# Optimization experiments

Measured on AMD Instinct MI355X. Metric: run time of the kernel, lower is better.

Reference implementation:

```python
import jax, jax.numpy as jnp
import numpy as np

B, S, D = 4, 4096, 2048
DH = D // 2
EPS = 1e-6


def setup_inputs() -> dict:
    key = jax.random.key(0)
    ks = jax.random.split(key, 6)
    return {
        "inputs": jax.random.normal(ks[0], (B * S, D), jnp.float32),
        "lf1_cache": jax.random.normal(ks[1], (B, D, 1, 1), jnp.float32),
        "lf2_cache": jax.random.normal(ks[2], (B, DH, 1, 1), jnp.float32),
        "w1": jax.random.normal(ks[3], (DH, D, 2), jnp.float32) / np.sqrt(2.0 * D).astype(np.float32),
        "b1": jnp.zeros((DH,), jnp.float32),
        "w2": jax.random.normal(ks[4], (D, DH, 2), jnp.float32) / np.sqrt(2.0 * DH).astype(np.float32),
        "b2": jnp.zeros((D,), jnp.float32),
        "ln_w": jnp.ones((D,), jnp.float32),
    }


def reference(inputs, lf1_cache, lf2_cache, w1, b1, w2, b2, ln_w):
    # inputs: [B*S, D] flat tokens; caches hold one previous timestep per batch.
    x = inputs.reshape(B, S, D)
    # prepend cached timestep -> [B, S+1, D]  (equiv. to torch.cat along conv time dim)
    x_cat = jnp.concatenate([lf1_cache[:, :, 0, 0][:, None, :], x], axis=1)
    # conv1: kernel size 2 over time, dense over channels (groups=1)
    # o1[b,t,e] = sum_d w1[e,d,0]*x_cat[b,t,d] + w1[e,d,1]*x_cat[b,t+1,d] + b1[e]
    o1 = (jnp.einsum('btd,ed->bte', x_cat[:, :-1], w1[:, :, 0])
          + jnp.einsum('btd,ed->bte', x_cat[:, 1:], w1[:, :, 1]) + b1)  # [B,S,DH]
    o1_cat = jnp.concatenate([lf2_cache[:, :, 0, 0][:, None, :], o1], axis=1)  # [B,S+1,DH]
    o2 = (jnp.einsum('bte,de->btd', o1_cat[:, :-1], w2[:, :, 0])
          + jnp.einsum('bte,de->btd', o1_cat[:, 1:], w2[:, :, 1]) + b2)  # [B,S,D]
    y = o2 + x  # residual add
    # RMSNorm over the channel dim
    inv_rms = jax.lax.rsqrt(jnp.mean(y * y, axis=-1, keepdims=True) + EPS)
    lf_output = y * inv_rms * ln_w  # [B, S, D]
    # new caches: last timestep of conv1 input and conv2 input, in [B,C,1,1] layout
    lf1 = x_cat[:, -1][:, :, None, None]
    lf2 = o1_cat[:, -1][:, :, None, None]
    return lf_output, lf1, lf2
```

## Files before the change

### kernel.cpp

```cpp
#include <hip/hip_runtime.h>
#include <cstdint>

#define BB 4
#define SS 4096
#define DD 2048
#define DH 1024
#define MM (BB * SS)
#define EPSV 1e-6f

typedef unsigned short u16;
typedef __bf16 bf16x8 __attribute__((ext_vector_type(8)));
typedef float f32x4 __attribute__((ext_vector_type(4)));


__device__ __forceinline__ u16 f2bf(float f) {
    uint32_t u = __float_as_uint(f);
    u += 0x7fffu + ((u >> 16) & 1u);
    return (u16)(u >> 16);
}

__device__ __forceinline__ void async16(const void* g, void* l) {
    __builtin_amdgcn_global_load_lds(
        (const __attribute__((address_space(1))) uint32_t*)g,
        (__attribute__((address_space(3))) uint32_t*)l,
        16, 0, 0);
}

#define FENCE asm volatile("" ::: "memory")


__global__ void cvt_f32_bf16(const float* __restrict__ in, u16* __restrict__ out, long n4) {
    long i = (long)blockIdx.x * blockDim.x + threadIdx.x;
    if (i >= n4) return;
    float4 v = *(const float4*)(in + i * 4);
    ushort4 o;
    o.x = f2bf(v.x); o.y = f2bf(v.y); o.z = f2bf(v.z); o.w = f2bf(v.w);
    *(ushort4*)(out + i * 4) = o;
}

__global__ void pack_w(const float* __restrict__ in, u16* __restrict__ out, int dshift) {
    int idx = blockIdx.x * 256 + threadIdx.x;
    int Dd = 1 << dshift;
    int e = idx >> dshift;
    int d = idx & (Dd - 1);
    float2 v = *(const float2*)(in + (long)idx * 2);
    long rowbase = (long)e * (Dd * 2);
    out[rowbase + d] = f2bf(v.x);
    out[rowbase + Dd + d] = f2bf(v.y);
}

template <int KD, int MODE>
__launch_bounds__(512, 2)
__global__ void gemm2tap(const u16* __restrict__ A,
                         const u16* __restrict__ cache,
                         const u16* __restrict__ Bt,
                         const float* __restrict__ bias,
                         u16* __restrict__ obf,
                         float* __restrict__ lf2out,
                         const float* __restrict__ xres,
                         float* __restrict__ yout)
{
    constexpr int KTOT = 2 * KD;
    constexpr int NT = KTOT / 64;
    constexpr int HALF_T = NT / 2;
    constexpr int NN = (MODE == 1) ? DH : DD;
    static_assert(NT >= 4 && (NT & 1) == 0, "tile schedule needs even NT >= 4");

    const int tid = threadIdx.x;
    const int lane = tid & 63;
    const int wave = tid >> 6;
    const int bm = blockIdx.x;
    const int bn = blockIdx.y;

    __shared__ __align__(16) u16 sm[65536];

    const int srow = wave * 16 + (lane >> 2);
    const int skc  = (lane & 3) ^ ((lane >> 3) & 3);
    const int sRowA = wave * 512;

    const u16 *aPrev0, *aPrev1, *aCur0, *aCur1, *bPtr0, *bPtr1;
    {
        long r0 = (long)bm * 256 + srow;
        long r1 = r0 + 128;
        aCur0 = A + r0 * KD + skc * 8;
        aCur1 = A + r1 * KD + skc * 8;
        aPrev0 = ((((int)r0) & (SS - 1)) == 0) ? (cache + (r0 >> 12) * KD + skc * 8)
                                               : (A + (r0 - 1) * KD + skc * 8);
        aPrev1 = ((((int)r1) & (SS - 1)) == 0) ? (cache + (r1 >> 12) * KD + skc * 8)
                                               : (A + (r1 - 1) * KD + skc * 8);
        long n0l = (long)bn * 256 + srow;
        bPtr0 = Bt + n0l * KTOT + skc * 8;
        bPtr1 = Bt + (n0l + 128) * KTOT + skc * 8;
    }

#define STAGE_A(DBUF_, TT_, KS_) do {                                          \
        const int _ko = (TT_) * 64 + (KS_) * 32;                               \
        const u16 *_g0, *_g1;                                                  \
        if ((TT_) < HALF_T) { _g0 = aPrev0 + _ko; _g1 = aPrev1 + _ko; }        \
        else { _g0 = aCur0 + (_ko - KD); _g1 = aCur1 + (_ko - KD); }           \
        async16(_g0, sm + (DBUF_) * 32768 + (KS_) * 8192 + sRowA);             \
        async16(_g1, sm + (DBUF_) * 32768 + (KS_) * 8192 + 4096 + sRowA);      \
    } while (0)

#define STAGE_B(DBUF_, TT_, KS_) do {                                          \
        const int _ko = (TT_) * 64 + (KS_) * 32;                               \
        async16(bPtr0 + _ko, sm + (DBUF_) * 32768 + 16384 + (KS_) * 8192 + sRowA);        \
        async16(bPtr1 + _ko, sm + (DBUF_) * 32768 + 16384 + (KS_) * 8192 + 4096 + sRowA); \
    } while (0)

    const int frow = lane & 15;
    const int fquad = lane >> 4;
    const int wm128 = (wave >> 2) * 128;
    const int wn64  = (wave & 3) * 64;
    const int fq8s = (fquad ^ ((frow >> 1) & 3)) * 8;
    const int afb = (wm128 + frow) * 32 + fq8s;
    const int bfb = (wn64 + frow) * 32 + fq8s;

    f32x4 acc[8][4];
#pragma unroll
    for (int i = 0; i < 8; ++i)
#pragma unroll
        for (int j = 0; j < 4; ++j)
            acc[i][j] = (f32x4){0.f, 0.f, 0.f, 0.f};

#define MFMA_(D_, A_, B_) D_ = __builtin_amdgcn_mfma_f32_16x16x32_bf16(A_, B_, D_, 0, 0, 0)

#define TILE2(T_, DB_, SP0_, SP1_, VM0S_, VM1S_)                               \
  {                                                                            \
    const u16* aro = sm + (DB_) * 32768;                                       \
    const u16* bro = aro + 16384;                                              \
    bf16x8 af[8], bq[4];                                                       \
                                   \
    _Pragma("unroll")                                                          \
    for (int mf = 0; mf < 8; ++mf)                                             \
        af[mf] = *(const bf16x8*)(aro + afb + mf * 512);                       \
    _Pragma("unroll")                                                          \
    for (int nf = 0; nf < 4; ++nf)                                             \
        bq[nf] = *(const bf16x8*)(bro + bfb + nf * 512);                       \
    if (SP0_) { STAGE_A((DB_) ^ 1, (T_) + 1, 1); STAGE_B((DB_) ^ 1, (T_) + 1, 1); } \
    FENCE; __builtin_amdgcn_s_barrier(); FENCE;                                \
    __builtin_amdgcn_s_setprio(1);                                             \
    _Pragma("unroll")                                                          \
    for (int mf = 0; mf < 8; ++mf)                                             \
        _Pragma("unroll")                                                      \
        for (int nf = 0; nf < 4; ++nf)                                         \
            MFMA_(acc[mf][nf], af[mf], bq[nf]);                                \
    __builtin_amdgcn_s_setprio(0);                                             \
    asm volatile(VM0S_ ::: "memory");                                          \
    __builtin_amdgcn_s_barrier(); FENCE;                                       \
                                   \
    _Pragma("unroll")                                                          \
    for (int mf = 0; mf < 8; ++mf)                                             \
        af[mf] = *(const bf16x8*)(aro + 8192 + afb + mf * 512);                \
    _Pragma("unroll")                                                          \
    for (int nf = 0; nf < 4; ++nf)                                             \
        bq[nf] = *(const bf16x8*)(bro + 8192 + bfb + nf * 512);                \
    if (SP1_) { STAGE_A((DB_), (T_) + 2, 0); STAGE_B((DB_), (T_) + 2, 0); }    \
    FENCE; __builtin_amdgcn_s_barrier(); FENCE;                                \
    __builtin_amdgcn_s_setprio(1);                                             \
    _Pragma("unroll")                                                          \
    for (int mf = 0; mf < 8; ++mf)                                             \
        _Pragma("unroll")                                                      \
        for (int nf = 0; nf < 4; ++nf)                                         \
            MFMA_(acc[mf][nf], af[mf], bq[nf]);                                \
    __builtin_amdgcn_s_setprio(0);                                             \
    asm volatile(VM1S_ ::: "memory");                                          \
    __builtin_amdgcn_s_barrier(); FENCE;                                       \
  }

    STAGE_A(0, 0, 0);
    STAGE_B(0, 0, 0);
    FENCE;
    STAGE_A(0, 0, 1);
    STAGE_B(0, 0, 1);
    STAGE_A(1, 1, 0);
    STAGE_B(1, 1, 0);
    asm volatile("s_waitcnt vmcnt(8)" ::: "memory");
    __builtin_amdgcn_s_barrier(); FENCE;

    for (int t = 0; t < NT - 2; t += 2) {
        TILE2(t,     0, 1, 1, "s_waitcnt vmcnt(8)", "s_waitcnt vmcnt(8)");
        TILE2(t + 1, 1, 1, 1, "s_waitcnt vmcnt(8)", "s_waitcnt vmcnt(8)");
    }
    TILE2(NT - 2, 0, 1, 0, "s_waitcnt vmcnt(8)", "s_waitcnt vmcnt(4)");
    TILE2(NT - 1, 1, 0, 0, "s_waitcnt vmcnt(0)", "s_waitcnt vmcnt(0)");

#undef TILE2
#undef STAGE_A
#undef STAGE_B

    const long m0 = (long)bm * 256 + wm128;
    const int n0 = bn * 256 + wn64;
#pragma unroll
    for (int mf = 0; mf < 8; ++mf) {
#pragma unroll
        for (int nf = 0; nf < 4; ++nf) {
            const int n = n0 + nf * 16 + frow;
            const float bv = bias[n];
#pragma unroll
            for (int v = 0; v < 4; ++v) {
                const long m = m0 + mf * 16 + fquad * 4 + v;
                float val = acc[mf][nf][v] + bv;
                if (MODE == 1) {
                    obf[m * NN + n] = f2bf(val);
                    if ((((int)m) & (SS - 1)) == (SS - 1))
                        lf2out[(m >> 12) * NN + n] = val;
                } else {
                    val += xres[m * NN + n];
                    yout[m * NN + n] = val;
                }
            }
        }
    }
}


__global__ void rmsnorm_inplace(float* __restrict__ y, const float* __restrict__ lnw) {
    const long r = blockIdx.x;
    float* row = y + r * DD;
    const int tid = threadIdx.x;

    float4 v0 = *(float4*)(row + tid * 4);
    float4 v1 = *(float4*)(row + 1024 + tid * 4);
    float s = v0.x * v0.x + v0.y * v0.y + v0.z * v0.z + v0.w * v0.w
            + v1.x * v1.x + v1.y * v1.y + v1.z * v1.z + v1.w * v1.w;
#pragma unroll
    for (int off = 32; off; off >>= 1) s += __shfl_xor(s, off, 64);

    __shared__ float red[4];
    if ((tid & 63) == 0) red[tid >> 6] = s;
    __syncthreads();
    float tot = red[0] + red[1] + red[2] + red[3];
    float inv = rsqrtf(tot * (1.0f / DD) + EPSV);

    float4 w0 = *(const float4*)(lnw + tid * 4);
    float4 w1 = *(const float4*)(lnw + 1024 + tid * 4);
    v0.x *= inv * w0.x; v0.y *= inv * w0.y; v0.z *= inv * w0.z; v0.w *= inv * w0.w;
    v1.x *= inv * w1.x; v1.y *= inv * w1.y; v1.z *= inv * w1.z; v1.w *= inv * w1.w;
    *(float4*)(row + tid * 4) = v0;
    *(float4*)(row + 1024 + tid * 4) = v1;
}

__global__ void lf1_copy(const float* __restrict__ x, float* __restrict__ out) {
    int idx = blockIdx.x * 256 + threadIdx.x;
    int b = idx >> 11;
    int d = idx & (DD - 1);
    out[idx] = x[((long)b * SS + (SS - 1)) * DD + d];
}


extern "C" void kernel_launch(void* const* d_in, const int* in_sizes, int n_in,
                              void* d_out, int out_size, void* d_ws, size_t ws_size,
                              hipStream_t stream) {
    const float* x    = (const float*)d_in[0];
    const float* lf1c = (const float*)d_in[1];
    const float* lf2c = (const float*)d_in[2];
    const float* w1   = (const float*)d_in[3];
    const float* b1   = (const float*)d_in[4];
    const float* w2   = (const float*)d_in[5];
    const float* b2   = (const float*)d_in[6];
    const float* lnw  = (const float*)d_in[7];

    float* out    = (float*)d_out;
    float* lf1out = out + (long)MM * DD;
    float* lf2out = lf1out + (long)BB * DD;

    char* ws = (char*)d_ws;
    u16* Xbf  = (u16*)ws; ws += (long)MM * DD * 2;
    u16* o1bf = (u16*)ws; ws += (long)MM * DH * 2;
    u16* W1b  = (u16*)ws; ws += (long)DH * (2 * DD) * 2;
    u16* W2b  = (u16*)ws; ws += (long)DD * (2 * DH) * 2;
    u16* c1   = (u16*)ws; ws += (long)BB * DD * 2;
    u16* c2   = (u16*)ws; ws += (long)BB * DH * 2;

    cvt_f32_bf16<<<32768, 256, 0, stream>>>(x, Xbf, (long)MM * DD / 4);
    cvt_f32_bf16<<<8, 256, 0, stream>>>(lf1c, c1, (long)BB * DD / 4);
    cvt_f32_bf16<<<4, 256, 0, stream>>>(lf2c, c2, (long)BB * DH / 4);
    pack_w<<<(DH * DD) / 256, 256, 0, stream>>>(w1, W1b, 11);
    pack_w<<<(DD * DH) / 256, 256, 0, stream>>>(w2, W2b, 10);

    gemm2tap<DD, 1><<<dim3(MM / 256, DH / 256), 512, 0, stream>>>(
        Xbf, c1, W1b, b1, o1bf, lf2out, nullptr, nullptr);

    gemm2tap<DH, 2><<<dim3(MM / 256, DD / 256), 512, 0, stream>>>(
        o1bf, c2, W2b, b2, nullptr, nullptr, x, out);

    rmsnorm_inplace<<<MM, 256, 0, stream>>>(out, lnw);
    lf1_copy<<<BB * DD / 256, 256, 0, stream>>>(x, lf1out);
}
```

Baseline: 571.0 us.

## Replace double-buffered K tiles with 4-slot ring pipeline, one barrier per step

Restructures the GEMM main loop from two 64-wide K tiles, each split into two 32-wide halves with two barriers per half, into a 4-slot ring of 32-wide K substeps. Each substep prefetches three substeps ahead and synchronises with a single barrier. This is meant to cut barrier count and deepen prefetch so more global-load latency hides behind MFMA work. It relies on careful vmcnt accounting; a wrong wait count could race on LDS slots.

```diff
diff --git a/kernel.cpp b/kernel.cpp
--- a/kernel.cpp
+++ b/kernel.cpp
@@ -62,9 +62,9 @@
 {
     constexpr int KTOT = 2 * KD;
     constexpr int NT = KTOT / 64;
-    constexpr int HALF_T = NT / 2;
+    constexpr int NS = 2 * NT;
     constexpr int NN = (MODE == 1) ? DH : DD;
-    static_assert(NT >= 4 && (NT & 1) == 0, "tile schedule needs even NT >= 4");
+    static_assert(NS % 4 == 0 && NS >= 8, "ring-4 schedule needs NS % 4 == 0, NS >= 8");
 
     const int tid = threadIdx.x;
     const int lane = tid & 63;
@@ -93,19 +93,15 @@
         bPtr1 = Bt + (n0l + 128) * KTOT + skc * 8;
     }
 
-#define STAGE_A(DBUF_, TT_, KS_) do {                                          \
-        const int _ko = (TT_) * 64 + (KS_) * 32;                               \
+#define STAGE(SLOT_, U_) do {                                                  \
+        const int _u = (U_);                                                   \
         const u16 *_g0, *_g1;                                                  \
-        if ((TT_) < HALF_T) { _g0 = aPrev0 + _ko; _g1 = aPrev1 + _ko; }        \
-        else { _g0 = aCur0 + (_ko - KD); _g1 = aCur1 + (_ko - KD); }           \
-        async16(_g0, sm + (DBUF_) * 32768 + (KS_) * 8192 + sRowA);             \
-        async16(_g1, sm + (DBUF_) * 32768 + (KS_) * 8192 + 4096 + sRowA);      \
-    } while (0)
-
-#define STAGE_B(DBUF_, TT_, KS_) do {                                          \
-        const int _ko = (TT_) * 64 + (KS_) * 32;                               \
-        async16(bPtr0 + _ko, sm + (DBUF_) * 32768 + 16384 + (KS_) * 8192 + sRowA);        \
-        async16(bPtr1 + _ko, sm + (DBUF_) * 32768 + 16384 + (KS_) * 8192 + 4096 + sRowA); \
+        if (_u < NT) { _g0 = aPrev0 + _u * 32; _g1 = aPrev1 + _u * 32; }       \
+        else { _g0 = aCur0 + (_u - NT) * 32; _g1 = aCur1 + (_u - NT) * 32; }   \
+        async16(_g0, sm + (SLOT_) * 8192 + sRowA);                             \
+        async16(_g1, sm + (SLOT_) * 8192 + 4096 + sRowA);                      \
+        async16(bPtr0 + _u * 32, sm + 32768 + (SLOT_) * 8192 + sRowA);         \
+        async16(bPtr1 + _u * 32, sm + 32768 + (SLOT_) * 8192 + 4096 + sRowA);  \
     } while (0)
 
     const int frow = lane & 15;
@@ -125,20 +121,18 @@
 
 #define MFMA_(D_, A_, B_) D_ = __builtin_amdgcn_mfma_f32_16x16x32_bf16(A_, B_, D_, 0, 0, 0)
 
-#define TILE2(T_, DB_, SP0_, SP1_, VM0S_, VM1S_)                               \
+#define STEP(SLOT_, U3_, DOSTG_, VMS_)                                         \
   {                                                                            \
-    const u16* aro = sm + (DB_) * 32768;                                       \
-    const u16* bro = aro + 16384;                                              \
-    bf16x8 af[8], bq[4];                                                       \
-                                   \
+    const u16* aro = sm + (SLOT_) * 8192;                                      \
+    const u16* bro = sm + 32768 + (SLOT_) * 8192;                              \
+    bf16x8 bq[4], af[8];                                                       \
+    _Pragma("unroll")                                                          \
+    for (int nf = 0; nf < 4; ++nf)                                             \
+        bq[nf] = *(const bf16x8*)(bro + bfb + nf * 512);                       \
     _Pragma("unroll")                                                          \
     for (int mf = 0; mf < 8; ++mf)                                             \
         af[mf] = *(const bf16x8*)(aro + afb + mf * 512);                       \
-    _Pragma("unroll")                                                          \
-    for (int nf = 0; nf < 4; ++nf)                                             \
-        bq[nf] = *(const bf16x8*)(bro + bfb + nf * 512);                       \
-    if (SP0_) { STAGE_A((DB_) ^ 1, (T_) + 1, 1); STAGE_B((DB_) ^ 1, (T_) + 1, 1); } \
-    FENCE; __builtin_amdgcn_s_barrier(); FENCE;                                \
+    if (DOSTG_) STAGE((((SLOT_) + 3) & 3), (U3_));                             \
     __builtin_amdgcn_s_setprio(1);                                             \
     _Pragma("unroll")                                                          \
     for (int mf = 0; mf < 8; ++mf)                                             \
@@ -146,48 +140,29 @@
         for (int nf = 0; nf < 4; ++nf)                                         \
             MFMA_(acc[mf][nf], af[mf], bq[nf]);                                \
     __builtin_amdgcn_s_setprio(0);                                             \
-    asm volatile(VM0S_ ::: "memory");                                          \
-    __builtin_amdgcn_s_barrier(); FENCE;                                       \
-                                   \
-    _Pragma("unroll")                                                          \
-    for (int mf = 0; mf < 8; ++mf)                                             \
-        af[mf] = *(const bf16x8*)(aro + 8192 + afb + mf * 512);                \
-    _Pragma("unroll")                                                          \
-    for (int nf = 0; nf < 4; ++nf)                                             \
-        bq[nf] = *(const bf16x8*)(bro + 8192 + bfb + nf * 512);                \
-    if (SP1_) { STAGE_A((DB_), (T_) + 2, 0); STAGE_B((DB_), (T_) + 2, 0); }    \
+    asm volatile(VMS_ ::: "memory");                                           \
     FENCE; __builtin_amdgcn_s_barrier(); FENCE;                                \
-    __builtin_amdgcn_s_setprio(1);                                             \
-    _Pragma("unroll")                                                          \
-    for (int mf = 0; mf < 8; ++mf)                                             \
-        _Pragma("unroll")                                                      \
-        for (int nf = 0; nf < 4; ++nf)                                         \
-            MFMA_(acc[mf][nf], af[mf], bq[nf]);                                \
-    __builtin_amdgcn_s_setprio(0);                                             \
-    asm volatile(VM1S_ ::: "memory");                                          \
-    __builtin_amdgcn_s_barrier(); FENCE;                                       \
   }
 
-    STAGE_A(0, 0, 0);
-    STAGE_B(0, 0, 0);
-    FENCE;
-    STAGE_A(0, 0, 1);
-    STAGE_B(0, 0, 1);
-    STAGE_A(1, 1, 0);
-    STAGE_B(1, 1, 0);
+    STAGE(0, 0); FENCE;
+    STAGE(1, 1); FENCE;
+    STAGE(2, 2);
     asm volatile("s_waitcnt vmcnt(8)" ::: "memory");
-    __builtin_amdgcn_s_barrier(); FENCE;
-
-    for (int t = 0; t < NT - 2; t += 2) {
-        TILE2(t,     0, 1, 1, "s_waitcnt vmcnt(8)", "s_waitcnt vmcnt(8)");
-        TILE2(t + 1, 1, 1, 1, "s_waitcnt vmcnt(8)", "s_waitcnt vmcnt(8)");
+    FENCE; __builtin_amdgcn_s_barrier(); FENCE;
+
+    for (int s = 0; s < NS - 4; s += 4) {
+        STEP(0, s + 3, 1, "s_waitcnt vmcnt(8)");
+        STEP(1, s + 4, 1, "s_waitcnt vmcnt(8)");
+        STEP(2, s + 5, 1, "s_waitcnt vmcnt(8)");
+        STEP(3, s + 6, 1, "s_waitcnt vmcnt(8)");
     }
-    TILE2(NT - 2, 0, 1, 0, "s_waitcnt vmcnt(8)", "s_waitcnt vmcnt(4)");
-    TILE2(NT - 1, 1, 0, 0, "s_waitcnt vmcnt(0)", "s_waitcnt vmcnt(0)");
-
-#undef TILE2
-#undef STAGE_A
-#undef STAGE_B
+    STEP(0, NS - 1, 1, "s_waitcnt vmcnt(8)");
+    STEP(1, 0, 0, "s_waitcnt vmcnt(4)");
+    STEP(2, 0, 0, "s_waitcnt vmcnt(0)");
+    STEP(3, 0, 0, "");
+
+#undef STEP
+#undef STAGE
 
     const long m0 = (long)bm * 256 + wm128;
     const int n0 = bn * 256 + wn64;
```

Result: faster. 555.4 us (-2.7%).
